# Performance work log

Measured on AMD Instinct MI355X. Metric: run time of the kernel, lower is better.

Reference implementation:

```python
import jax, jax.numpy as jnp
import numpy as np

NUM_EXPERT = 8
TOP_K = 1


def setup_inputs() -> dict:
    key = jax.random.key(0)
    ks = jax.random.split(key, 6)
    B, S, D, E, F = 8, 2048, 768, 8, 469
    scale = 0.02
    return {
        "x": jax.random.normal(ks[0], (B, S, D), dtype=jnp.float32),
        "Wg": jax.random.normal(ks[1], (E, D), dtype=jnp.float32) * scale,
        "bg": jnp.zeros((E,), dtype=jnp.float32),
        "W1": jax.random.normal(ks[2], (E, F, D), dtype=jnp.float32) * scale,
        "W2": jax.random.normal(ks[3], (E, F, D), dtype=jnp.float32) * scale,
        "W3": jax.random.normal(ks[4], (E, D, F), dtype=jnp.float32) * scale,
    }


def reference(x, Wg, bg, W1, W2, W3):
    # x: [B, S, D]; Wg: [E, D]; W1/W2: [E, F, D] (torch Linear layout [out,in]); W3: [E, D, F]
    B, S, D = x.shape
    E = Wg.shape[0]
    xf = x.reshape(B * S, D)  # [T, D]

    # gating: top-k over expert logits, softmax over the selected logits
    gate = xf @ Wg.T + bg  # [T, E]
    vals, idx = jax.lax.top_k(gate, TOP_K)  # [T, K]
    probs = jax.nn.softmax(vals, axis=-1)  # [T, K] (all ones for K=1)

    # combine weights per (token, expert): sum over k slots of onehot * prob
    dispatch = jnp.sum(
        jax.nn.one_hot(idx, E, dtype=x.dtype) * probs[..., None], axis=1
    )  # [T, E]

    # dense grouped SwiGLU FFN over all experts, combined by dispatch weights
    h = jax.nn.silu(jnp.einsum("td,efd->tef", xf, W1)) * jnp.einsum(
        "td,efd->tef", xf, W2
    )  # [T, E, F]
    out = jnp.einsum("tef,edf,te->td", h, W3, dispatch)  # [T, D]
    return out.reshape(B, S, D)
```

## Files before the change

### kernel.cpp

```cpp
#include <hip/hip_runtime.h>
#include <hip/hip_bf16.h>
#include <stdint.h>

#define TT 16384
#define DD 768
#define EE 8
#define FF 469
#define FP 512
#define NCHUNK (TT / 64)
#define MAXTILES 136

typedef __attribute__((ext_vector_type(8))) short s16x8;
typedef __attribute__((ext_vector_type(4))) float f32x4;

__device__ __forceinline__ ushort f2bf(float f) {
  uint32_t u = __builtin_bit_cast(uint32_t, f);
  u += 0x7fffu + ((u >> 16) & 1u);
  return (ushort)(u >> 16);
}

__device__ __forceinline__ void gload16(const void* g, void* l) {
  __builtin_amdgcn_global_load_lds((const __attribute__((address_space(1))) unsigned int*)g,
                                   (__attribute__((address_space(3))) unsigned int*)l,
                                   16, 0, 0);
}

__global__ __launch_bounds__(256) void gate_conv_kernel(
    const float* __restrict__ x, const float* __restrict__ Wg,
    const float* __restrict__ bg, int* __restrict__ eidx,
    ushort* __restrict__ xbf) {
  __shared__ float4 wgs[EE * DD / 4];
  int tid = threadIdx.x;
  for (int i = tid; i < EE * DD / 4; i += 256) wgs[i] = ((const float4*)Wg)[i];
  __syncthreads();

  int t = blockIdx.x * 4 + (tid >> 6);
  int lane = tid & 63;
  const float4* xr = (const float4*)(x + (size_t)t * DD);
  float4 xv[3];
#pragma unroll
  for (int k = 0; k < 3; ++k) xv[k] = xr[lane + 64 * k];

  float acc[EE];
#pragma unroll
  for (int e = 0; e < EE; ++e) acc[e] = 0.f;
#pragma unroll
  for (int k = 0; k < 3; ++k) {
#pragma unroll
    for (int e = 0; e < EE; ++e) {
      float4 w = wgs[e * 192 + lane + 64 * k];
      acc[e] += xv[k].x * w.x + xv[k].y * w.y + xv[k].z * w.z + xv[k].w * w.w;
    }
  }

  uint2* xd = (uint2*)(xbf + (size_t)t * DD);
#pragma unroll
  for (int k = 0; k < 3; ++k) {
    union { ushort u[4]; uint2 w; } p;
    p.u[0] = f2bf(xv[k].x); p.u[1] = f2bf(xv[k].y);
    p.u[2] = f2bf(xv[k].z); p.u[3] = f2bf(xv[k].w);
    xd[lane + 64 * k] = p.w;
  }

#pragma unroll
  for (int off = 32; off; off >>= 1) {
#pragma unroll
    for (int e = 0; e < EE; ++e) acc[e] += __shfl_down(acc[e], off);
  }
  if (lane == 0) {
    float best = acc[0] + bg[0];
    int bi = 0;
#pragma unroll
    for (int e = 1; e < EE; ++e) {
      float v = acc[e] + bg[e];
      if (v > best) { best = v; bi = e; }
    }
    eidx[t] = bi;
  }
}

__global__ void hist_kernel(const int* __restrict__ eidx, int* __restrict__ cnt) {
  int c = blockIdx.x * 4 + (threadIdx.x >> 6);
  int lane = threadIdx.x & 63;
  int v = eidx[c * 64 + lane];
#pragma unroll
  for (int e = 0; e < EE; ++e) {
    unsigned long long me = __ballot(v == e);
    if (lane == 0) cnt[e * NCHUNK + c] = __popcll(me);
  }
}

__global__ void scan_kernel(const int* __restrict__ cnt, int* __restrict__ scanEx,
                            int* __restrict__ offs, int* __restrict__ tileE,
                            int* __restrict__ tileT0) {
  int e = threadIdx.x >> 6;
  int lane = threadIdx.x & 63;
  __shared__ int totals[EE];
  int carry = 0;
#pragma unroll
  for (int g = 0; g < NCHUNK / 64; ++g) {
    int v = cnt[e * NCHUNK + g * 64 + lane];
    int s = v;
#pragma unroll
    for (int d = 1; d < 64; d <<= 1) {
      int t = __shfl_up(s, d);
      if (lane >= d) s += t;
    }
    scanEx[e * NCHUNK + g * 64 + lane] = carry + s - v;
    carry += __shfl(s, 63);
  }
  if (lane == 0) totals[e] = carry;
  __syncthreads();
  if (threadIdx.x == 0) {
    int s = 0;
    for (int e2 = 0; e2 < EE; ++e2) { offs[e2] = s; s += totals[e2]; }
    offs[EE] = s;
    int idx = 0;
    for (int e2 = 0; e2 < EE; ++e2) {
      int nt = (totals[e2] + 127) >> 7;
      for (int j = 0; j < nt; ++j) { tileE[idx] = e2; tileT0[idx] = j << 7; ++idx; }
    }
    for (; idx < MAXTILES; ++idx) tileE[idx] = -1;
  }
}

__global__ void scatter2_kernel(const int* __restrict__ eidx, const int* __restrict__ offs,
                                const int* __restrict__ scanEx, int* __restrict__ perm) {
  int c = blockIdx.x * 4 + (threadIdx.x >> 6);
  int lane = threadIdx.x & 63;
  int t = c * 64 + lane;
  int v = eidx[t];
  unsigned long long mym = 0;
#pragma unroll
  for (int e = 0; e < EE; ++e) {
    unsigned long long me = __ballot(v == e);
    if (v == e) mym = me;
  }
  int rank = __popcll(mym & ((1ULL << lane) - 1ULL));
  perm[offs[v] + scanEx[v * NCHUNK + c] + rank] = t;
}

__global__ void convw12_kernel(const float* __restrict__ W1, const float* __restrict__ W2,
                               ushort* __restrict__ w12b) {
  const int n4 = EE * 2 * FP * (DD / 4);
  for (int i = blockIdx.x * blockDim.x + threadIdx.x; i < n4; i += gridDim.x * blockDim.x) {
    int d4 = i % (DD / 4);
    int er = i / (DD / 4);
    int row = er & 1023;
    int e = er >> 10;
    int f = row >> 1;
    union { ushort u[4]; uint2 w; } p;
    if (f < FF) {
      const float* src = ((row & 1) ? W2 : W1) + ((size_t)e * FF + f) * DD;
      float4 v = ((const float4*)src)[d4];
      p.u[0] = f2bf(v.x); p.u[1] = f2bf(v.y); p.u[2] = f2bf(v.z); p.u[3] = f2bf(v.w);
    } else {
      p.w.x = 0u; p.w.y = 0u;
    }
    ((uint2*)w12b)[i] = p.w;
  }
}

__global__ void convw3_kernel(const float* __restrict__ W3, ushort* __restrict__ w3b) {
  const int n = EE * DD * FP;
  for (int i = blockIdx.x * blockDim.x + threadIdx.x; i < n; i += gridDim.x * blockDim.x) {
    int f = i % FP;
    int ed = i / FP;
    float v = (f < FF) ? W3[(size_t)ed * FF + f] : 0.f;
    w3b[i] = f2bf(v);
  }
}

__global__ __launch_bounds__(256) void ffn1_kernel(
    const ushort* __restrict__ xbf, const ushort* __restrict__ w12b,
    const int* __restrict__ perm, const int* __restrict__ offs,
    const int* __restrict__ tileE, const int* __restrict__ tileT0,
    ushort* __restrict__ hbf) {
  int bid = blockIdx.x;
  int L = (bid & 7) * MAXTILES + (bid >> 3);
  int ti = L >> 3;
  int y = L & 7;
  int e = tileE[ti];
  if (e < 0) return;
  int tile0 = tileT0[ti];
  int gOff = offs[e];
  int Ne = offs[e + 1] - gOff;
  int n0 = y * 128;

  __shared__ __align__(16) short As[2][128 * 32];
  __shared__ __align__(16) short Bs[2][128 * 32];

  int tid = threadIdx.x;
  int w = tid >> 6, lane = tid & 63;
  int lr = lane >> 2, lg = lane & 3;

  int r0 = w * 32 + lr, r1 = r0 + 16;
  int g0 = lg ^ ((r0 >> 1) & 3);
  int g1 = lg ^ ((r1 >> 1) & 3);
  int last = gOff + Ne - 1;
  int tok0 = perm[min(gOff + tile0 + r0, last)];
  int tok1 = perm[min(gOff + tile0 + r1, last)];
  const ushort* asrc0 = xbf + (size_t)tok0 * DD + g0 * 8;
  const ushort* asrc1 = xbf + (size_t)tok1 * DD + g1 * 8;
  const ushort* bsrc0 = w12b + ((size_t)(e << 10) + n0 + r0) * DD + g0 * 8;
  const ushort* bsrc1 = w12b + ((size_t)(e << 10) + n0 + r1) * DD + g1 * 8;
  int sdst0 = (w * 32) * 32;
  int sdst1 = sdst0 + 16 * 32;

  int wr = w >> 1, wc = w & 1;
  int lrow = lane & 15, kh = lane >> 4;
  int aoff[4], boff[4];
#pragma unroll
  for (int m = 0; m < 4; ++m) {
    int ra = wr * 64 + m * 16 + lrow;
    aoff[m] = ra * 32 + (kh ^ ((ra >> 1) & 3)) * 8;
    int rb = wc * 64 + m * 16 + lrow;
    boff[m] = rb * 32 + (kh ^ ((rb >> 1) & 3)) * 8;
  }

  f32x4 acc[4][4];
  f32x4 zero = {0.f, 0.f, 0.f, 0.f};
#pragma unroll
  for (int m = 0; m < 4; ++m)
#pragma unroll
    for (int n = 0; n < 4; ++n) acc[m][n] = zero;

  gload16(asrc0, &As[0][sdst0]);
  gload16(asrc1, &As[0][sdst1]);
  gload16(bsrc0, &Bs[0][sdst0]);
  gload16(bsrc1, &Bs[0][sdst1]);
  __syncthreads();

  const int NT = DD / 32;
  for (int t = 0; t < NT; ++t) {
    int cur = t & 1;
    if (t + 1 < NT) {
      int k = (t + 1) * 32;
      gload16(asrc0 + k, &As[cur ^ 1][sdst0]);
      gload16(asrc1 + k, &As[cur ^ 1][sdst1]);
      gload16(bsrc0 + k, &Bs[cur ^ 1][sdst0]);
      gload16(bsrc1 + k, &Bs[cur ^ 1][sdst1]);
    }
    s16x8 af[4], bfr[4];
#pragma unroll
    for (int m = 0; m < 4; ++m) af[m] = *(const s16x8*)&As[cur][aoff[m]];
#pragma unroll
    for (int n = 0; n < 4; ++n) bfr[n] = *(const s16x8*)&Bs[cur][boff[n]];
#pragma unroll
    for (int m = 0; m < 4; ++m)
#pragma unroll
      for (int n = 0; n < 4; ++n)
        acc[m][n] = __builtin_amdgcn_mfma_f32_16x16x32_bf16(af[m], bfr[n], acc[m][n], 0, 0, 0);
    __syncthreads();
  }

#pragma unroll
  for (int m = 0; m < 4; ++m) {
    int rbase = tile0 + wr * 64 + m * 16 + kh * 4;
#pragma unroll
    for (int n = 0; n < 4; ++n) {
      int f = (n0 + wc * 64 + n * 16 + lrow) >> 1;
#pragma unroll
      for (int r = 0; r < 4; ++r) {
        float val = acc[m][n][r];
        float par = __shfl_xor(val, 1);
        float u = (lane & 1) ? par : val;
        float vv = (lane & 1) ? val : par;
        float h = (u / (1.f + __expf(-u))) * vv;
        int gr = rbase + r;
        if (!(lane & 1) && gr < Ne)
          hbf[(size_t)(gOff + gr) * FP + f] = f2bf(h);
      }
    }
  }
}

__global__ __launch_bounds__(256) void ffn2_kernel(
    const ushort* __restrict__ hbf, const ushort* __restrict__ w3b,
    const int* __restrict__ perm, const int* __restrict__ offs,
    const int* __restrict__ tileE, const int* __restrict__ tileT0,
    float* __restrict__ out) {
  int bid = blockIdx.x;
  int L = (bid & 7) * 102 + (bid >> 3);
  int ti = L / 6;
  int y = L % 6;
  int e = tileE[ti];
  if (e < 0) return;
  int tile0 = tileT0[ti];
  int gOff = offs[e];
  int Ne = offs[e + 1] - gOff;
  int d0 = y * 128;

  __shared__ __align__(16) short As[2][128 * 32];
  __shared__ __align__(16) short Bs[2][128 * 32];

  int tid = threadIdx.x;
  int w = tid >> 6, lane = tid & 63;
  int lr = lane >> 2, lg = lane & 3;

  int r0 = w * 32 + lr, r1 = r0 + 16;
  int g0 = lg ^ ((r0 >> 1) & 3);
  int g1 = lg ^ ((r1 >> 1) & 3);
  int last = gOff + Ne - 1;
  const ushort* asrc0 = hbf + (size_t)min(gOff + tile0 + r0, last) * FP + g0 * 8;
  const ushort* asrc1 = hbf + (size_t)min(gOff + tile0 + r1, last) * FP + g1 * 8;
  const ushort* bsrc0 = w3b + ((size_t)e * DD + d0 + r0) * FP + g0 * 8;
  const ushort* bsrc1 = w3b + ((size_t)e * DD + d0 + r1) * FP + g1 * 8;
  int sdst0 = (w * 32) * 32;
  int sdst1 = sdst0 + 16 * 32;

  int wr = w >> 1, wc = w & 1;
  int lrow = lane & 15, kh = lane >> 4;
  int aoff[4], boff[4];
#pragma unroll
  for (int m = 0; m < 4; ++m) {
    int ra = wr * 64 + m * 16 + lrow;
    aoff[m] = ra * 32 + (kh ^ ((ra >> 1) & 3)) * 8;
    int rb = wc * 64 + m * 16 + lrow;
    boff[m] = rb * 32 + (kh ^ ((rb >> 1) & 3)) * 8;
  }

  f32x4 acc[4][4];
  f32x4 zero = {0.f, 0.f, 0.f, 0.f};
#pragma unroll
  for (int m = 0; m < 4; ++m)
#pragma unroll
    for (int n = 0; n < 4; ++n) acc[m][n] = zero;

  gload16(asrc0, &As[0][sdst0]);
  gload16(asrc1, &As[0][sdst1]);
  gload16(bsrc0, &Bs[0][sdst0]);
  gload16(bsrc1, &Bs[0][sdst1]);
  __syncthreads();

  const int NT = FP / 32;
  for (int t = 0; t < NT; ++t) {
    int cur = t & 1;
    if (t + 1 < NT) {
      int k = (t + 1) * 32;
      gload16(asrc0 + k, &As[cur ^ 1][sdst0]);
      gload16(asrc1 + k, &As[cur ^ 1][sdst1]);
      gload16(bsrc0 + k, &Bs[cur ^ 1][sdst0]);
      gload16(bsrc1 + k, &Bs[cur ^ 1][sdst1]);
    }
    s16x8 af[4], bfr[4];
#pragma unroll
    for (int m = 0; m < 4; ++m) af[m] = *(const s16x8*)&As[cur][aoff[m]];
#pragma unroll
    for (int n = 0; n < 4; ++n) bfr[n] = *(const s16x8*)&Bs[cur][boff[n]];
#pragma unroll
    for (int m = 0; m < 4; ++m)
#pragma unroll
      for (int n = 0; n < 4; ++n)
        acc[m][n] = __builtin_amdgcn_mfma_f32_16x16x32_bf16(af[m], bfr[n], acc[m][n], 0, 0, 0);
    __syncthreads();
  }

#pragma unroll
  for (int m = 0; m < 4; ++m) {
#pragma unroll
    for (int r = 0; r < 4; ++r) {
      int gr = tile0 + wr * 64 + m * 16 + kh * 4 + r;
      if (gr < Ne) {
        int t = perm[gOff + gr];
        float* orow = out + (size_t)t * DD + d0 + wc * 64;
#pragma unroll
        for (int n = 0; n < 4; ++n) orow[n * 16 + lrow] = acc[m][n][r];
      }
    }
  }
}

extern "C" void kernel_launch(void* const* d_in, const int* in_sizes, int n_in,
                              void* d_out, int out_size, void* d_ws, size_t ws_size,
                              hipStream_t stream) {
  const float* x = (const float*)d_in[0];
  const float* Wg = (const float*)d_in[1];
  const float* bg = (const float*)d_in[2];
  const float* W1 = (const float*)d_in[3];
  const float* W2 = (const float*)d_in[4];
  const float* W3 = (const float*)d_in[5];
  float* out = (float*)d_out;

  char* ws = (char*)d_ws;
  int* eidx = (int*)ws;
  int* perm = (int*)(ws + 65536);
  int* offs = (int*)(ws + 131072);
  int* cnt = (int*)(ws + 131072 + 128);
  int* scanEx = (int*)(ws + 131072 + 128 + 8192);
  int* tileE = (int*)(ws + 131072 + 128 + 16384);
  int* tileT0 = tileE + MAXTILES + 8;
  ushort* xbf = (ushort*)(ws + 262144);
  ushort* w12b = xbf + (size_t)TT * DD;
  ushort* w3b = w12b + (size_t)EE * 2 * FP * DD;
  ushort* hbf = w3b + (size_t)EE * DD * FP;

  gate_conv_kernel<<<TT / 4, 256, 0, stream>>>(x, Wg, bg, eidx, xbf);
  convw12_kernel<<<2048, 256, 0, stream>>>(W1, W2, w12b);
  convw3_kernel<<<2048, 256, 0, stream>>>(W3, w3b);
  hist_kernel<<<NCHUNK / 4, 256, 0, stream>>>(eidx, cnt);
  scan_kernel<<<1, 512, 0, stream>>>(cnt, scanEx, offs, tileE, tileT0);
  scatter2_kernel<<<NCHUNK / 4, 256, 0, stream>>>(eidx, offs, scanEx, perm);
  ffn1_kernel<<<8 * MAXTILES, 256, 0, stream>>>(xbf, w12b, perm, offs, tileE, tileT0, hbf);
  ffn2_kernel<<<6 * MAXTILES, 256, 0, stream>>>(hbf, w3b, perm, offs, tileE, tileT0, out);
}
```

Measured before the change: 121.5 us.

## Triple-buffer LDS tiles with one barrier per k-step in both FFN GEMMs

Both grouped GEMM kernels move from double to triple LDS buffering and prefetch two k-tiles ahead. The loop now uses an explicit vmcnt wait and a single s_barrier per iteration instead of two __syncthreads, and raises wave priority around the MFMA block. The goal is to hide global-to-LDS load latency and cut barrier stalls. In exchange, LDS use grows from 32KB to 48KB per block, which may lower occupancy, and the hand-written vmcnt counts must match the number of outstanding loads for the result to be correct.

```diff
diff --git a/kernel.cpp b/kernel.cpp
--- a/kernel.cpp
+++ b/kernel.cpp
@@ -187,8 +187,8 @@
   int Ne = offs[e + 1] - gOff;
   int n0 = y * 128;
 
-  __shared__ __align__(16) short As[2][128 * 32];
-  __shared__ __align__(16) short Bs[2][128 * 32];
+  __shared__ __align__(16) short As[3][128 * 32];
+  __shared__ __align__(16) short Bs[3][128 * 32];
 
   int tid = threadIdx.x;
   int w = tid >> 6, lane = tid & 63;
@@ -229,29 +229,39 @@
   gload16(asrc1, &As[0][sdst1]);
   gload16(bsrc0, &Bs[0][sdst0]);
   gload16(bsrc1, &Bs[0][sdst1]);
-  __syncthreads();
+  gload16(asrc0 + 32, &As[1][sdst0]);
+  gload16(asrc1 + 32, &As[1][sdst1]);
+  gload16(bsrc0 + 32, &Bs[1][sdst0]);
+  gload16(bsrc1 + 32, &Bs[1][sdst1]);
 
   const int NT = DD / 32;
+#pragma unroll
   for (int t = 0; t < NT; ++t) {
-    int cur = t & 1;
-    if (t + 1 < NT) {
-      int k = (t + 1) * 32;
-      gload16(asrc0 + k, &As[cur ^ 1][sdst0]);
-      gload16(asrc1 + k, &As[cur ^ 1][sdst1]);
-      gload16(bsrc0 + k, &Bs[cur ^ 1][sdst0]);
-      gload16(bsrc1 + k, &Bs[cur ^ 1][sdst1]);
+    const int cur = t % 3;
+    if (t < NT - 1) asm volatile("s_waitcnt vmcnt(4)" ::: "memory");
+    else            asm volatile("s_waitcnt vmcnt(0)" ::: "memory");
+    __builtin_amdgcn_s_barrier();
+    __builtin_amdgcn_sched_barrier(0);
+    if (t + 2 < NT) {
+      const int nb = (t + 2) % 3;
+      int k = (t + 2) * 32;
+      gload16(asrc0 + k, &As[nb][sdst0]);
+      gload16(asrc1 + k, &As[nb][sdst1]);
+      gload16(bsrc0 + k, &Bs[nb][sdst0]);
+      gload16(bsrc1 + k, &Bs[nb][sdst1]);
     }
     s16x8 af[4], bfr[4];
 #pragma unroll
     for (int m = 0; m < 4; ++m) af[m] = *(const s16x8*)&As[cur][aoff[m]];
 #pragma unroll
     for (int n = 0; n < 4; ++n) bfr[n] = *(const s16x8*)&Bs[cur][boff[n]];
+    __builtin_amdgcn_s_setprio(1);
 #pragma unroll
     for (int m = 0; m < 4; ++m)
 #pragma unroll
       for (int n = 0; n < 4; ++n)
         acc[m][n] = __builtin_amdgcn_mfma_f32_16x16x32_bf16(af[m], bfr[n], acc[m][n], 0, 0, 0);
-    __syncthreads();
+    __builtin_amdgcn_s_setprio(0);
   }
 
 #pragma unroll
@@ -291,8 +301,8 @@
   int Ne = offs[e + 1] - gOff;
   int d0 = y * 128;
 
-  __shared__ __align__(16) short As[2][128 * 32];
-  __shared__ __align__(16) short Bs[2][128 * 32];
+  __shared__ __align__(16) short As[3][128 * 32];
+  __shared__ __align__(16) short Bs[3][128 * 32];
 
   int tid = threadIdx.x;
   int w = tid >> 6, lane = tid & 63;
@@ -331,29 +341,39 @@
   gload16(asrc1, &As[0][sdst1]);
   gload16(bsrc0, &Bs[0][sdst0]);
   gload16(bsrc1, &Bs[0][sdst1]);
-  __syncthreads();
+  gload16(asrc0 + 32, &As[1][sdst0]);
+  gload16(asrc1 + 32, &As[1][sdst1]);
+  gload16(bsrc0 + 32, &Bs[1][sdst0]);
+  gload16(bsrc1 + 32, &Bs[1][sdst1]);
 
   const int NT = FP / 32;
+#pragma unroll
   for (int t = 0; t < NT; ++t) {
-    int cur = t & 1;
-    if (t + 1 < NT) {
-      int k = (t + 1) * 32;
-      gload16(asrc0 + k, &As[cur ^ 1][sdst0]);
-      gload16(asrc1 + k, &As[cur ^ 1][sdst1]);
-      gload16(bsrc0 + k, &Bs[cur ^ 1][sdst0]);
-      gload16(bsrc1 + k, &Bs[cur ^ 1][sdst1]);
+    const int cur = t % 3;
+    if (t < NT - 1) asm volatile("s_waitcnt vmcnt(4)" ::: "memory");
+    else            asm volatile("s_waitcnt vmcnt(0)" ::: "memory");
+    __builtin_amdgcn_s_barrier();
+    __builtin_amdgcn_sched_barrier(0);
+    if (t + 2 < NT) {
+      const int nb = (t + 2) % 3;
+      int k = (t + 2) * 32;
+      gload16(asrc0 + k, &As[nb][sdst0]);
+      gload16(asrc1 + k, &As[nb][sdst1]);
+      gload16(bsrc0 + k, &Bs[nb][sdst0]);
+      gload16(bsrc1 + k, &Bs[nb][sdst1]);
     }
     s16x8 af[4], bfr[4];
 #pragma unroll
     for (int m = 0; m < 4; ++m) af[m] = *(const s16x8*)&As[cur][aoff[m]];
 #pragma unroll
     for (int n = 0; n < 4; ++n) bfr[n] = *(const s16x8*)&Bs[cur][boff[n]];
+    __builtin_amdgcn_s_setprio(1);
 #pragma unroll
     for (int m = 0; m < 4; ++m)
 #pragma unroll
       for (int n = 0; n < 4; ++n)
         acc[m][n] = __builtin_amdgcn_mfma_f32_16x16x32_bf16(af[m], bfr[n], acc[m][n], 0, 0, 0);
-    __syncthreads();
+    __builtin_amdgcn_s_setprio(0);
   }
 
 #pragma unroll
```

After: 122.6 us. About the same (+0.9%).

## Fuse histogram into gating, merge weight casts, and retune GEMM mainloop sync

Applied to the files above, without the earlier changes.

Per-chunk expert counts are now built with atomics inside the gating kernel, after a memset, so the separate histogram kernel is gone. The two weight-conversion kernels are merged into one launch, and the W3 cast now writes four outputs per thread. Both FFN GEMM mainloops are fully unrolled and use a single top-of-loop barrier, explicit vmcnt waits and MFMA priority raising, replacing two __syncthreads per iteration. The aim is fewer launches and less synchronization stall. The risk is that without a barrier after the wait, other waves' LDS-direct loads may not be visible when fragments are read.

```diff
diff --git a/kernel.cpp b/kernel.cpp
--- a/kernel.cpp
+++ b/kernel.cpp
@@ -28,7 +28,7 @@
 __global__ __launch_bounds__(256) void gate_conv_kernel(
     const float* __restrict__ x, const float* __restrict__ Wg,
     const float* __restrict__ bg, int* __restrict__ eidx,
-    ushort* __restrict__ xbf) {
+    ushort* __restrict__ xbf, int* __restrict__ cnt) {
   __shared__ float4 wgs[EE * DD / 4];
   int tid = threadIdx.x;
   for (int i = tid; i < EE * DD / 4; i += 256) wgs[i] = ((const float4*)Wg)[i];
@@ -76,17 +76,7 @@
       if (v > best) { best = v; bi = e; }
     }
     eidx[t] = bi;
-  }
-}
-
-__global__ void hist_kernel(const int* __restrict__ eidx, int* __restrict__ cnt) {
-  int c = blockIdx.x * 4 + (threadIdx.x >> 6);
-  int lane = threadIdx.x & 63;
-  int v = eidx[c * 64 + lane];
-#pragma unroll
-  for (int e = 0; e < EE; ++e) {
-    unsigned long long me = __ballot(v == e);
-    if (lane == 0) cnt[e * NCHUNK + c] = __popcll(me);
+    atomicAdd(&cnt[bi * NCHUNK + (t >> 6)], 1);
   }
 }
 
@@ -140,34 +130,40 @@
   perm[offs[v] + scanEx[v * NCHUNK + c] + rank] = t;
 }
 
-__global__ void convw12_kernel(const float* __restrict__ W1, const float* __restrict__ W2,
-                               ushort* __restrict__ w12b) {
-  const int n4 = EE * 2 * FP * (DD / 4);
-  for (int i = blockIdx.x * blockDim.x + threadIdx.x; i < n4; i += gridDim.x * blockDim.x) {
-    int d4 = i % (DD / 4);
-    int er = i / (DD / 4);
-    int row = er & 1023;
-    int e = er >> 10;
-    int f = row >> 1;
-    union { ushort u[4]; uint2 w; } p;
-    if (f < FF) {
-      const float* src = ((row & 1) ? W2 : W1) + ((size_t)e * FF + f) * DD;
-      float4 v = ((const float4*)src)[d4];
-      p.u[0] = f2bf(v.x); p.u[1] = f2bf(v.y); p.u[2] = f2bf(v.z); p.u[3] = f2bf(v.w);
+#define N12 (EE * 2 * FP * (DD / 4))
+#define N3  (EE * DD * (FP / 4))
+__global__ void convw_kernel(const float* __restrict__ W1, const float* __restrict__ W2,
+                             const float* __restrict__ W3, ushort* __restrict__ w12b,
+                             ushort* __restrict__ w3b) {
+  for (int i = blockIdx.x * blockDim.x + threadIdx.x; i < N12 + N3;
+       i += gridDim.x * blockDim.x) {
+    if (i < N12) {
+      int d4 = i % (DD / 4);
+      int er = i / (DD / 4);
+      int row = er & 1023;
+      int e = er >> 10;
+      int f = row >> 1;
+      union { ushort u[4]; uint2 w; } p;
+      if (f < FF) {
+        const float* src = ((row & 1) ? W2 : W1) + ((size_t)e * FF + f) * DD;
+        float4 v = ((const float4*)src)[d4];
+        p.u[0] = f2bf(v.x); p.u[1] = f2bf(v.y); p.u[2] = f2bf(v.z); p.u[3] = f2bf(v.w);
+      } else {
+        p.w.x = 0u; p.w.y = 0u;
+      }
+      ((uint2*)w12b)[i] = p.w;
     } else {
-      p.w.x = 0u; p.w.y = 0u;
-    }
-    ((uint2*)w12b)[i] = p.w;
-  }
-}
-
-__global__ void convw3_kernel(const float* __restrict__ W3, ushort* __restrict__ w3b) {
-  const int n = EE * DD * FP;
-  for (int i = blockIdx.x * blockDim.x + threadIdx.x; i < n; i += gridDim.x * blockDim.x) {
-    int f = i % FP;
-    int ed = i / FP;
-    float v = (f < FF) ? W3[(size_t)ed * FF + f] : 0.f;
-    w3b[i] = f2bf(v);
+      int j = i - N12;
+      int f4 = (j % (FP / 4)) * 4;
+      int ed = j / (FP / 4);
+      union { ushort u[4]; uint2 w; } p;
+#pragma unroll
+      for (int q = 0; q < 4; ++q) {
+        int f = f4 + q;
+        p.u[q] = (f < FF) ? f2bf(W3[(size_t)ed * FF + f]) : (ushort)0;
+      }
+      ((uint2*)w3b)[(size_t)ed * (FP / 4) + (f4 >> 2)] = p.w;
+    }
   }
 }
 
@@ -229,29 +225,36 @@
   gload16(asrc1, &As[0][sdst1]);
   gload16(bsrc0, &Bs[0][sdst0]);
   gload16(bsrc1, &Bs[0][sdst1]);
-  __syncthreads();
 
   const int NT = DD / 32;
+#pragma unroll
   for (int t = 0; t < NT; ++t) {
-    int cur = t & 1;
+    const int cur = t & 1;
+    __builtin_amdgcn_s_barrier();
+    __builtin_amdgcn_sched_barrier(0);
     if (t + 1 < NT) {
       int k = (t + 1) * 32;
       gload16(asrc0 + k, &As[cur ^ 1][sdst0]);
       gload16(asrc1 + k, &As[cur ^ 1][sdst1]);
       gload16(bsrc0 + k, &Bs[cur ^ 1][sdst0]);
       gload16(bsrc1 + k, &Bs[cur ^ 1][sdst1]);
-    }
+      asm volatile("s_waitcnt vmcnt(4)" ::: "memory");
+    } else {
+      asm volatile("s_waitcnt vmcnt(0)" ::: "memory");
+    }
+    __builtin_amdgcn_sched_barrier(0);
     s16x8 af[4], bfr[4];
 #pragma unroll
     for (int m = 0; m < 4; ++m) af[m] = *(const s16x8*)&As[cur][aoff[m]];
 #pragma unroll
     for (int n = 0; n < 4; ++n) bfr[n] = *(const s16x8*)&Bs[cur][boff[n]];
+    __builtin_amdgcn_s_setprio(1);
 #pragma unroll
     for (int m = 0; m < 4; ++m)
 #pragma unroll
       for (int n = 0; n < 4; ++n)
         acc[m][n] = __builtin_amdgcn_mfma_f32_16x16x32_bf16(af[m], bfr[n], acc[m][n], 0, 0, 0);
-    __syncthreads();
+    __builtin_amdgcn_s_setprio(0);
   }
 
 #pragma unroll
@@ -331,29 +334,36 @@
   gload16(asrc1, &As[0][sdst1]);
   gload16(bsrc0, &Bs[0][sdst0]);
   gload16(bsrc1, &Bs[0][sdst1]);
-  __syncthreads();
 
   const int NT = FP / 32;
+#pragma unroll
   for (int t = 0; t < NT; ++t) {
-    int cur = t & 1;
+    const int cur = t & 1;
+    __builtin_amdgcn_s_barrier();
+    __builtin_amdgcn_sched_barrier(0);
     if (t + 1 < NT) {
       int k = (t + 1) * 32;
       gload16(asrc0 + k, &As[cur ^ 1][sdst0]);
       gload16(asrc1 + k, &As[cur ^ 1][sdst1]);
       gload16(bsrc0 + k, &Bs[cur ^ 1][sdst0]);
       gload16(bsrc1 + k, &Bs[cur ^ 1][sdst1]);
-    }
+      asm volatile("s_waitcnt vmcnt(4)" ::: "memory");
+    } else {
+      asm volatile("s_waitcnt vmcnt(0)" ::: "memory");
+    }
+    __builtin_amdgcn_sched_barrier(0);
     s16x8 af[4], bfr[4];
 #pragma unroll
     for (int m = 0; m < 4; ++m) af[m] = *(const s16x8*)&As[cur][aoff[m]];
 #pragma unroll
     for (int n = 0; n < 4; ++n) bfr[n] = *(const s16x8*)&Bs[cur][boff[n]];
+    __builtin_amdgcn_s_setprio(1);
 #pragma unroll
     for (int m = 0; m < 4; ++m)
 #pragma unroll
       for (int n = 0; n < 4; ++n)
         acc[m][n] = __builtin_amdgcn_mfma_f32_16x16x32_bf16(af[m], bfr[n], acc[m][n], 0, 0, 0);
-    __syncthreads();
+    __builtin_amdgcn_s_setprio(0);
   }
 
 #pragma unroll
@@ -395,12 +405,11 @@
   ushort* w3b = w12b + (size_t)EE * 2 * FP * DD;
   ushort* hbf = w3b + (size_t)EE * DD * FP;
 
-  gate_conv_kernel<<<TT / 4, 256, 0, stream>>>(x, Wg, bg, eidx, xbf);
-  convw12_kernel<<<2048, 256, 0, stream>>>(W1, W2, w12b);
-  convw3_kernel<<<2048, 256, 0, stream>>>(W3, w3b);
-  hist_kernel<<<NCHUNK / 4, 256, 0, stream>>>(eidx, cnt);
+  hipMemsetAsync(cnt, 0, EE * NCHUNK * 4, stream);
+  gate_conv_kernel<<<TT / 4, 256, 0, stream>>>(x, Wg, bg, eidx, xbf, cnt);
+  convw_kernel<<<2048, 256, 0, stream>>>(W1, W2, W3, w12b, w3b);
   scan_kernel<<<1, 512, 0, stream>>>(cnt, scanEx, offs, tileE, tileT0);
   scatter2_kernel<<<NCHUNK / 4, 256, 0, stream>>>(eidx, offs, scanEx, perm);
   ffn1_kernel<<<8 * MAXTILES, 256, 0, stream>>>(xbf, w12b, perm, offs, tileE, tileT0, hbf);
-  ffn2_kernel<<<6 * MAXTILES, 256, 0, stream>>>(hbf, w3b, perm, offs, tileE, tileT0, out);
-}
+  ffn2_kernel<<<8 * 102, 256, 0, stream>>>(hbf, w3b, perm, offs, tileE, tileT0, out);
+}
```

Result: slower. 126.0 us (+3.7%).
